# Kernel optimization log

Hardware: AMD Instinct MI355X
Metric: run time of the kernel (lower is better)

Reference implementation:

```python
import jax, jax.numpy as jnp
import numpy as np

N, M, NB, NA, NT, T, U = 1024, 32, 1024, 1536, 2048, 6, 32

def _one_hot_bool(n, m):
    ids = (jnp.arange(n) * m) // n  # contiguous assignment of entities to molecules
    return (jax.nn.one_hot(ids, m, dtype=jnp.float32) > 0.5)

def setup_inputs() -> dict:
    key = jax.random.key(0)
    ks = jax.random.split(key, 32)
    nrm = lambda i, shape, s=1.0: jax.random.normal(ks[i], shape, dtype=jnp.float32) * s
    inp = {
        'h_v': nrm(0, (N, U)), 'h_e': nrm(1, (NB, U)), 'h_a': nrm(2, (NA, U)),
        'h_t': nrm(3, (NT, U)), 'h_u': nrm(4, (M, U)),
        'h_v_history': nrm(5, (N, T, U)), 'h_e_history': nrm(6, (NB, T, U)),
        'h_a_history': nrm(7, (NA, T, U)), 'h_t_history': nrm(8, (NT, T, U)),
        'h_u_history': nrm(9, (M, T, U)),
        'atom_in_mol': _one_hot_bool(N, M), 'bond_in_mol': _one_hot_bool(NB, M),
        'angle_in_mol': _one_hot_bool(NA, M), 'torsion_in_mol': _one_hot_bool(NT, M),
        'adjacency_map': nrm(10, (N, N)), 'coordinates': nrm(11, (N, 3), 3.0),
        # learned parameters
        'Wk': nrm(12, (U, U), 0.1), 'bk': jnp.zeros((U,), jnp.float32),
        'Wq': nrm(13, (U, U), 0.1), 'bq': jnp.zeros((U,), jnp.float32),
        'Wv0': nrm(14, (1, U), 0.1), 'bv0': jnp.zeros((U,), jnp.float32),
        'Wv1': nrm(15, (U, U), 0.1), 'bv1': jnp.zeros((U,), jnp.float32),
        'Wp0': nrm(16, (3 * U, U), 0.1), 'bp0': jnp.zeros((U,), jnp.float32),
        'Wp1': nrm(17, (U, 19), 0.1), 'bp1': jnp.zeros((19,), jnp.float32),
        'Wd0': nrm(18, (5 * T * U, 64), 0.1), 'bd0': jnp.zeros((64,), jnp.float32),
        'Wd1': nrm(19, (64, 64), 0.1), 'bd1': jnp.zeros((64,), jnp.float32),
        'Wd2': nrm(20, (64, 19), 0.1), 'bd2': jnp.zeros((19,), jnp.float32),
    }
    return inp

def reference(h_v, h_e, h_a, h_t, h_u, h_v_history, h_e_history, h_a_history,
              h_t_history, h_u_history, atom_in_mol, bond_in_mol, angle_in_mol,
              torsion_in_mol, adjacency_map, coordinates,
              Wk, bk, Wq, bq, Wv0, bv0, Wv1, bv1, Wp0, bp0, Wp1, bp1,
              Wd0, bd0, Wd1, bd1, Wd2, bd2):
    A = atom_in_mol.astype(jnp.float32)              # [N, M]
    per_mol_mask = A @ A.T                           # [N, N] block-diagonal 0/1
    # pairwise Euclidean distance matrix
    diff = coordinates[:, None, :] - coordinates[None, :, :]
    dist = jnp.sqrt(jnp.maximum(jnp.sum(diff * diff, -1), 1e-12))[..., None]  # [N, N, 1]
    mask3 = per_mol_mask[..., None]                  # [N, N, 1]
    v = mask3 * (jax.nn.elu(dist @ Wv0 + bv0) @ Wv1 + bv1)          # [N, N, U]
    k = mask3 * (h_v @ Wk + bk)[:, None, :]                          # [N, N, U]
    q = mask3 * (h_v @ Wq + bq)[None, :, :]                          # [N, N, U]
    h_pair = jnp.concatenate([k, q, v], axis=2)                      # [N, N, 3U]
    h_pair = jnp.sum(jax.nn.sigmoid(h_pair @ Wp0 + bp0) @ Wp1 + bp1, axis=0)  # [N, 19]
    h_pair = A.T @ h_pair                                            # [M, 19]
    # per-mol segment sums of histories (faithful to mask-multiply-reduce, as einsum)
    seg = lambda mask, hist: jnp.einsum('em,etu->mtu', mask.astype(jnp.float32), hist)
    h_v_bar = seg(atom_in_mol, h_v_history).reshape(M, T * U)
    h_e_bar = seg(bond_in_mol, h_e_history).reshape(M, T * U)
    h_a_bar = seg(angle_in_mol, h_a_history).reshape(M, T * U)
    h_t_bar = seg(torsion_in_mol, h_t_history).reshape(M, T * U)  # computed, unused (as in source)
    # ConcatenateThenFullyConnect((64,'sigmoid',64,19)); note h_a_bar passed twice per source
    x = jnp.concatenate([h_v_bar, h_e_bar, h_u_history.reshape(M, T * U), h_a_bar, h_a_bar], axis=1)
    y = (jax.nn.sigmoid(x @ Wd0 + bd0) @ Wd1 + bd1) @ Wd2 + bd2      # [M, 19]
    return y + h_pair
```

## Files before the change

### kernel.cpp

```cpp
#include <hip/hip_runtime.h>
#include <math.h>


__device__ __forceinline__ float sigmoidf_(float x) { return 1.0f / (1.0f + __expf(-x)); }

__global__ __launch_bounds__(256) void fused_kernel(
    const float* __restrict__ h_v,
    const float* __restrict__ coords,
    const float* __restrict__ Wk, const float* __restrict__ bk,
    const float* __restrict__ Wq, const float* __restrict__ bq,
    const float* __restrict__ Wv0, const float* __restrict__ bv0,
    const float* __restrict__ Wv1, const float* __restrict__ bv1,
    const float* __restrict__ Wp0, const float* __restrict__ bp0,
    const float* __restrict__ Wp1, const float* __restrict__ bp1,
    const float* __restrict__ hvh,
    const float* __restrict__ heh,
    const float* __restrict__ hah,
    const float* __restrict__ huh,
    const float* __restrict__ Wd0, const float* __restrict__ bd0,
    const float* __restrict__ Wd1, const float* __restrict__ bd1,
    const float* __restrict__ Wd2, const float* __restrict__ bd2,
    float* __restrict__ out)
{
    __shared__ float hl[1024];
    __shared__ float wkl[1024], wql[1024], wv1l[1024];
    __shared__ float wp0l[3072];
    __shared__ float Kl[32 * 36], Ql[32 * 36];
    __shared__ float SKl[32 * 36], SQl[32 * 36];
    __shared__ float W2l[1024];
    __shared__ float wp1l[608];
    __shared__ float cbl[32], wv0l[32], bv0l[32];
    __shared__ float cxl[32], cyl[32], czl[32];
    __shared__ float Gl[4 * 32];
    __shared__ float Gs[32];
    __shared__ float xpart[14 * 192];
    __shared__ float xl[960];
    __shared__ float hp[4 * 64];
    __shared__ float h0[64], h1[64];

    const int tid = threadIdx.x;
    const int b = blockIdx.x;

    if (b < 32) {
        const int m = b;
        for (int task = tid; task < 672; task += 256) {
            const int seg = task / 48, c4 = task % 48;
            const float* src; int row0;
            if (seg < 4)      { src = hvh + (size_t)(m * 32) * 192; row0 = seg * 8; }
            else if (seg < 8) { src = heh + (size_t)(m * 32) * 192; row0 = (seg - 4) * 8; }
            else              { src = hah + (size_t)(m * 48) * 192; row0 = (seg - 8) * 8; }
            float4 acc = {0, 0, 0, 0};
            #pragma unroll
            for (int r = 0; r < 8; ++r) {
                const float4 v = *(const float4*)(src + (size_t)(row0 + r) * 192 + c4 * 4);
                acc.x += v.x; acc.y += v.y; acc.z += v.z; acc.w += v.w;
            }
            *(float4*)&xpart[seg * 192 + c4 * 4] = acc;
        }
        __syncthreads();
        if (tid < 192) {
            const float sv = xpart[tid] + xpart[192 + tid] + xpart[384 + tid] + xpart[576 + tid];
            const float se = xpart[768 + tid] + xpart[960 + tid] + xpart[1152 + tid] + xpart[1344 + tid];
            float sa = 0.0f;
            #pragma unroll
            for (int s2 = 8; s2 < 14; ++s2) sa += xpart[s2 * 192 + tid];
            xl[tid]       = sv;
            xl[192 + tid] = se;
            xl[384 + tid] = huh[m * 192 + tid];
            xl[576 + tid] = sa;
            xl[768 + tid] = sa;
        }
        __syncthreads();
        {
            const int o2 = tid & 63, part = tid >> 6;
            const int k0 = part * 240;
            float ssum = 0.0f;
            #pragma unroll 8
            for (int k = k0; k < k0 + 240; ++k) ssum += xl[k] * Wd0[k * 64 + o2];
            hp[part * 64 + o2] = ssum;
        }
        __syncthreads();
        if (tid < 64)
            h0[tid] = sigmoidf_(hp[tid] + hp[64 + tid] + hp[128 + tid] + hp[192 + tid] + bd0[tid]);
        __syncthreads();
        if (tid < 64) {
            float ssum = bd1[tid];
            #pragma unroll
            for (int k = 0; k < 64; ++k) ssum += h0[k] * Wd1[k * 64 + tid];
            h1[tid] = ssum;
        }
        __syncthreads();
        if (tid < 19) {
            float y = bd2[tid];
            #pragma unroll
            for (int k = 0; k < 64; ++k) y += h1[k] * Wd2[k * 19 + tid];
            float c0m = 0.0f;
            for (int u = 0; u < 32; ++u) c0m += sigmoidf_(bp0[u]) * Wp1[u * 19 + tid];
            atomicAdd(&out[m * 19 + tid], y + 31744.0f * c0m + 32768.0f * bp1[tid]);
        }
        return;
    }

    const int bb = b - 32;
    const int mol = bb >> 3;
    const int o = bb & 7;
    const int base = mol * 32;

    ((float4*)hl)[tid]   = ((const float4*)(h_v + (size_t)base * 32))[tid];
    ((float4*)wkl)[tid]  = ((const float4*)Wk)[tid];
    ((float4*)wql)[tid]  = ((const float4*)Wq)[tid];
    ((float4*)wv1l)[tid] = ((const float4*)Wv1)[tid];
    ((float4*)wp0l)[tid]       = ((const float4*)Wp0)[tid];
    ((float4*)wp0l)[tid + 256] = ((const float4*)Wp0)[tid + 256];
    ((float4*)wp0l)[tid + 512] = ((const float4*)Wp0)[tid + 512];
    for (int i = tid; i < 608; i += 256) wp1l[i] = Wp1[i];
    if (tid < 32) {
        wv0l[tid] = Wv0[tid];
        bv0l[tid] = bv0[tid];
        const int gi = base + tid;
        cxl[tid] = coords[gi * 3 + 0];
        cyl[tid] = coords[gi * 3 + 1];
        czl[tid] = coords[gi * 3 + 2];
    }
    __syncthreads();

    {
        const int u = tid & 31, g = tid >> 5;
        const int a0 = g * 4;
        float ka[4], qa[4];
        #pragma unroll
        for (int j = 0; j < 4; ++j) { ka[j] = bk[u]; qa[j] = bq[u]; }
        #pragma unroll
        for (int t4 = 0; t4 < 32; t4 += 4) {
            float4 h0v = *(const float4*)&hl[(a0 + 0) * 32 + t4];
            float4 h1v = *(const float4*)&hl[(a0 + 1) * 32 + t4];
            float4 h2v = *(const float4*)&hl[(a0 + 2) * 32 + t4];
            float4 h3v = *(const float4*)&hl[(a0 + 3) * 32 + t4];
            #pragma unroll
            for (int i = 0; i < 4; ++i) {
                const float wk = wkl[(t4 + i) * 32 + u];
                const float wq = wql[(t4 + i) * 32 + u];
                const float e0 = (&h0v.x)[i], e1 = (&h1v.x)[i], e2 = (&h2v.x)[i], e3 = (&h3v.x)[i];
                ka[0] += e0 * wk; ka[1] += e1 * wk; ka[2] += e2 * wk; ka[3] += e3 * wk;
                qa[0] += e0 * wq; qa[1] += e1 * wq; qa[2] += e2 * wq; qa[3] += e3 * wq;
            }
        }
        #pragma unroll
        for (int j = 0; j < 4; ++j) {
            Kl[(a0 + j) * 36 + u] = ka[j];
            Ql[(a0 + j) * 36 + u] = qa[j];
        }
    }
    __syncthreads();

    {
        const int w = tid & 31, g = tid >> 5;
        const int a0 = g * 4;
        float sk[4] = {0, 0, 0, 0}, sq[4] = {0, 0, 0, 0}, w2[4] = {0, 0, 0, 0};
        #pragma unroll
        for (int u4 = 0; u4 < 32; u4 += 4) {
            float4 k0 = *(const float4*)&Kl[(a0 + 0) * 36 + u4];
            float4 k1 = *(const float4*)&Kl[(a0 + 1) * 36 + u4];
            float4 k2 = *(const float4*)&Kl[(a0 + 2) * 36 + u4];
            float4 k3 = *(const float4*)&Kl[(a0 + 3) * 36 + u4];
            float4 q0 = *(const float4*)&Ql[(a0 + 0) * 36 + u4];
            float4 q1 = *(const float4*)&Ql[(a0 + 1) * 36 + u4];
            float4 q2 = *(const float4*)&Ql[(a0 + 2) * 36 + u4];
            float4 q3 = *(const float4*)&Ql[(a0 + 3) * 36 + u4];
            float4 v0 = *(const float4*)&wv1l[(a0 + 0) * 32 + u4];
            float4 v1 = *(const float4*)&wv1l[(a0 + 1) * 32 + u4];
            float4 v2 = *(const float4*)&wv1l[(a0 + 2) * 32 + u4];
            float4 v3 = *(const float4*)&wv1l[(a0 + 3) * 32 + u4];
            #pragma unroll
            for (int i = 0; i < 4; ++i) {
                const float pk = wp0l[(u4 + i) * 32 + w];
                const float pq = wp0l[(32 + u4 + i) * 32 + w];
                const float pv = wp0l[(64 + u4 + i) * 32 + w];
                sk[0] += (&k0.x)[i] * pk; sk[1] += (&k1.x)[i] * pk;
                sk[2] += (&k2.x)[i] * pk; sk[3] += (&k3.x)[i] * pk;
                sq[0] += (&q0.x)[i] * pq; sq[1] += (&q1.x)[i] * pq;
                sq[2] += (&q2.x)[i] * pq; sq[3] += (&q3.x)[i] * pq;
                w2[0] += (&v0.x)[i] * pv; w2[1] += (&v1.x)[i] * pv;
                w2[2] += (&v2.x)[i] * pv; w2[3] += (&v3.x)[i] * pv;
            }
        }
        #pragma unroll
        for (int j = 0; j < 4; ++j) {
            SKl[(a0 + j) * 36 + w] = sk[j];
            SQl[(a0 + j) * 36 + w] = sq[j];
            W2l[(a0 + j) * 32 + w] = w2[j];
        }
    }
    if (tid < 32) {
        float s = bp0[tid];
        #pragma unroll
        for (int u = 0; u < 32; ++u) s += bv1[u] * wp0l[(64 + u) * 32 + tid];
        cbl[tid] = s;
    }
    __syncthreads();

    const int ts = tid >> 2, sub = tid & 3;
    const int c0 = sub * 8;

    float g[8] = {0, 0, 0, 0, 0, 0, 0, 0};

    auto slot_accum = [&](int i, int j, bool mir) {
        const float dx = cxl[i] - cxl[j];
        const float dy = cyl[i] - cyl[j];
        const float dz = czl[i] - czl[j];
        const float dist = sqrtf(fmaxf(dx * dx + dy * dy + dz * dz, 1e-12f));
        float ew[8];
        {
            const float4 ca = *(const float4*)&cbl[c0];
            const float4 cb = *(const float4*)&cbl[c0 + 4];
            #pragma unroll
            for (int k = 0; k < 4; ++k) { ew[k] = (&ca.x)[k]; ew[k + 4] = (&cb.x)[k]; }
        }
        #pragma unroll
        for (int t = 0; t < 32; ++t) {
            const float xx = dist * wv0l[t] + bv0l[t];
            const float e = (xx > 0.0f) ? xx : (__expf(xx) - 1.0f);
            const float4 wa = *(const float4*)&W2l[t * 32 + c0];
            const float4 wb = *(const float4*)&W2l[t * 32 + c0 + 4];
            #pragma unroll
            for (int k = 0; k < 4; ++k) {
                ew[k]     += e * (&wa.x)[k];
                ew[k + 4] += e * (&wb.x)[k];
            }
        }
        {
            const float4 ka = *(const float4*)&SKl[i * 36 + c0];
            const float4 kb = *(const float4*)&SKl[i * 36 + c0 + 4];
            const float4 qa = *(const float4*)&SQl[j * 36 + c0];
            const float4 qb = *(const float4*)&SQl[j * 36 + c0 + 4];
            #pragma unroll
            for (int k = 0; k < 4; ++k) {
                g[k]     += sigmoidf_(ew[k]     + (&ka.x)[k] + (&qa.x)[k]);
                g[k + 4] += sigmoidf_(ew[k + 4] + (&kb.x)[k] + (&qb.x)[k]);
            }
        }
        if (mir) {
            const float4 ka = *(const float4*)&SKl[j * 36 + c0];
            const float4 kb = *(const float4*)&SKl[j * 36 + c0 + 4];
            const float4 qa = *(const float4*)&SQl[i * 36 + c0];
            const float4 qb = *(const float4*)&SQl[i * 36 + c0 + 4];
            #pragma unroll
            for (int k = 0; k < 4; ++k) {
                g[k]     += sigmoidf_(ew[k]     + (&ka.x)[k] + (&qa.x)[k]);
                g[k + 4] += sigmoidf_(ew[k + 4] + (&kb.x)[k] + (&qb.x)[k]);
            }
        }
    };

    {
        const int row = ts >> 5;
        const int i = ts & 31;
        int d; bool mir;
        if (o < 7) { d = 2 * o + 1 + row; mir = true; }
        else       { d = (row == 0) ? 15 : 16; mir = (row == 0); }
        const int j = (i + d) & 31;
        slot_accum(i, j, mir);
    }
    if (o == 7 && tid < 128) {
        const int i = tid >> 2;
        slot_accum(i, i, false);
    }

    #pragma unroll
    for (int k = 0; k < 8; ++k) {
        g[k] += __shfl_xor(g[k], 4);
        g[k] += __shfl_xor(g[k], 8);
        g[k] += __shfl_xor(g[k], 16);
        g[k] += __shfl_xor(g[k], 32);
    }
    const int lane = tid & 63, wid = tid >> 6;
    if (lane < 4) {
        #pragma unroll
        for (int k = 0; k < 8; ++k) Gl[wid * 32 + sub * 8 + k] = g[k];
    }
    __syncthreads();
    if (tid < 32) Gs[tid] = Gl[tid] + Gl[32 + tid] + Gl[64 + tid] + Gl[96 + tid];
    __syncthreads();
    if (tid < 19) {
        float r = 0.0f;
        #pragma unroll
        for (int u = 0; u < 32; ++u) r += Gs[u] * wp1l[u * 19 + tid];
        atomicAdd(&out[mol * 19 + tid], r);
    }
}

extern "C" void kernel_launch(void* const* d_in, const int* in_sizes, int n_in,
                              void* d_out, int out_size, void* d_ws, size_t ws_size,
                              hipStream_t stream) {
    (void)in_sizes; (void)n_in; (void)d_ws; (void)ws_size;
    const float* h_v    = (const float*)d_in[0];
    const float* hvh    = (const float*)d_in[5];
    const float* heh    = (const float*)d_in[6];
    const float* hah    = (const float*)d_in[7];
    const float* huh    = (const float*)d_in[9];
    const float* coords = (const float*)d_in[15];
    const float* Wk  = (const float*)d_in[16]; const float* bk  = (const float*)d_in[17];
    const float* Wq  = (const float*)d_in[18]; const float* bq  = (const float*)d_in[19];
    const float* Wv0 = (const float*)d_in[20]; const float* bv0 = (const float*)d_in[21];
    const float* Wv1 = (const float*)d_in[22]; const float* bv1 = (const float*)d_in[23];
    const float* Wp0 = (const float*)d_in[24]; const float* bp0 = (const float*)d_in[25];
    const float* Wp1 = (const float*)d_in[26]; const float* bp1 = (const float*)d_in[27];
    const float* Wd0 = (const float*)d_in[28]; const float* bd0 = (const float*)d_in[29];
    const float* Wd1 = (const float*)d_in[30]; const float* bd1 = (const float*)d_in[31];
    const float* Wd2 = (const float*)d_in[32]; const float* bd2 = (const float*)d_in[33];

    hipMemsetAsync(d_out, 0, (size_t)out_size * sizeof(float), stream);
    fused_kernel<<<288, 256, 0, stream>>>(h_v, coords, Wk, bk, Wq, bq,
                                          Wv0, bv0, Wv1, bv1, Wp0, bp0, Wp1, bp1,
                                          hvh, heh, hah, huh,
                                          Wd0, bd0, Wd1, bd1, Wd2, bd2,
                                          (float*)d_out);
}
```

Before: 24.53 us.

## Merge per-molecule work into one 1024-thread block, drop memset and atomics

Work is redistributed from 288 blocks of 256 threads (32 MLP blocks plus 8 pair blocks per molecule) to 32 blocks of 1024 threads, one per molecule. History segment sums, K/Q projection and the pairwise sigmoid stage now run inside the same block. Each thread processes 4 pairs plus their mirror pairs, and the diagonal term is computed separately with a 1e-6 distance. Because the block writes its output directly, the memset and the atomicAdds are no longer needed. In exchange, only 32 CUs are used, and the larger blocks may add register pressure and longer serial tails in the MLP stage.

```diff
diff --git a/kernel.cpp b/kernel.cpp
--- a/kernel.cpp
+++ b/kernel.cpp
@@ -4,7 +4,7 @@
 
 __device__ __forceinline__ float sigmoidf_(float x) { return 1.0f / (1.0f + __expf(-x)); }
 
-__global__ __launch_bounds__(256) void fused_kernel(
+__global__ __launch_bounds__(1024) void fused32(
     const float* __restrict__ h_v,
     const float* __restrict__ coords,
     const float* __restrict__ Wk, const float* __restrict__ bk,
@@ -28,92 +28,25 @@
     __shared__ float Kl[32 * 36], Ql[32 * 36];
     __shared__ float SKl[32 * 36], SQl[32 * 36];
     __shared__ float W2l[1024];
-    __shared__ float wp1l[608];
     __shared__ float cbl[32], wv0l[32], bv0l[32];
     __shared__ float cxl[32], cyl[32], czl[32];
-    __shared__ float Gl[4 * 32];
+    __shared__ float Gl[8 * 32];
     __shared__ float Gs[32];
     __shared__ float xpart[14 * 192];
     __shared__ float xl[960];
-    __shared__ float hp[4 * 64];
+    __shared__ float hp[16 * 64];
     __shared__ float h0[64], h1[64];
 
     const int tid = threadIdx.x;
-    const int b = blockIdx.x;
-
-    if (b < 32) {
-        const int m = b;
-        for (int task = tid; task < 672; task += 256) {
-            const int seg = task / 48, c4 = task % 48;
-            const float* src; int row0;
-            if (seg < 4)      { src = hvh + (size_t)(m * 32) * 192; row0 = seg * 8; }
-            else if (seg < 8) { src = heh + (size_t)(m * 32) * 192; row0 = (seg - 4) * 8; }
-            else              { src = hah + (size_t)(m * 48) * 192; row0 = (seg - 8) * 8; }
-            float4 acc = {0, 0, 0, 0};
-            #pragma unroll
-            for (int r = 0; r < 8; ++r) {
-                const float4 v = *(const float4*)(src + (size_t)(row0 + r) * 192 + c4 * 4);
-                acc.x += v.x; acc.y += v.y; acc.z += v.z; acc.w += v.w;
-            }
-            *(float4*)&xpart[seg * 192 + c4 * 4] = acc;
-        }
-        __syncthreads();
-        if (tid < 192) {
-            const float sv = xpart[tid] + xpart[192 + tid] + xpart[384 + tid] + xpart[576 + tid];
-            const float se = xpart[768 + tid] + xpart[960 + tid] + xpart[1152 + tid] + xpart[1344 + tid];
-            float sa = 0.0f;
-            #pragma unroll
-            for (int s2 = 8; s2 < 14; ++s2) sa += xpart[s2 * 192 + tid];
-            xl[tid]       = sv;
-            xl[192 + tid] = se;
-            xl[384 + tid] = huh[m * 192 + tid];
-            xl[576 + tid] = sa;
-            xl[768 + tid] = sa;
-        }
-        __syncthreads();
-        {
-            const int o2 = tid & 63, part = tid >> 6;
-            const int k0 = part * 240;
-            float ssum = 0.0f;
-            #pragma unroll 8
-            for (int k = k0; k < k0 + 240; ++k) ssum += xl[k] * Wd0[k * 64 + o2];
-            hp[part * 64 + o2] = ssum;
-        }
-        __syncthreads();
-        if (tid < 64)
-            h0[tid] = sigmoidf_(hp[tid] + hp[64 + tid] + hp[128 + tid] + hp[192 + tid] + bd0[tid]);
-        __syncthreads();
-        if (tid < 64) {
-            float ssum = bd1[tid];
-            #pragma unroll
-            for (int k = 0; k < 64; ++k) ssum += h0[k] * Wd1[k * 64 + tid];
-            h1[tid] = ssum;
-        }
-        __syncthreads();
-        if (tid < 19) {
-            float y = bd2[tid];
-            #pragma unroll
-            for (int k = 0; k < 64; ++k) y += h1[k] * Wd2[k * 19 + tid];
-            float c0m = 0.0f;
-            for (int u = 0; u < 32; ++u) c0m += sigmoidf_(bp0[u]) * Wp1[u * 19 + tid];
-            atomicAdd(&out[m * 19 + tid], y + 31744.0f * c0m + 32768.0f * bp1[tid]);
-        }
-        return;
-    }
-
-    const int bb = b - 32;
-    const int mol = bb >> 3;
-    const int o = bb & 7;
-    const int base = mol * 32;
-
-    ((float4*)hl)[tid]   = ((const float4*)(h_v + (size_t)base * 32))[tid];
-    ((float4*)wkl)[tid]  = ((const float4*)Wk)[tid];
-    ((float4*)wql)[tid]  = ((const float4*)Wq)[tid];
-    ((float4*)wv1l)[tid] = ((const float4*)Wv1)[tid];
-    ((float4*)wp0l)[tid]       = ((const float4*)Wp0)[tid];
-    ((float4*)wp0l)[tid + 256] = ((const float4*)Wp0)[tid + 256];
-    ((float4*)wp0l)[tid + 512] = ((const float4*)Wp0)[tid + 512];
-    for (int i = tid; i < 608; i += 256) wp1l[i] = Wp1[i];
+    const int m = blockIdx.x;
+    const int base = m * 32;
+
+    if (tid < 256)                       ((float4*)hl)[tid]         = ((const float4*)(h_v + (size_t)base * 32))[tid];
+    else if (tid < 512)                  ((float4*)wkl)[tid - 256]  = ((const float4*)Wk)[tid - 256];
+    else if (tid < 768)                  ((float4*)wql)[tid - 512]  = ((const float4*)Wq)[tid - 512];
+    else                                 ((float4*)wv1l)[tid - 768] = ((const float4*)Wv1)[tid - 768];
+    if (tid < 768)                       ((float4*)wp0l)[tid]       = ((const float4*)Wp0)[tid];
+    else if (tid < 816)                  ((float4*)(xl + 384))[tid - 768] = ((const float4*)(huh + (size_t)m * 192))[tid - 768];
     if (tid < 32) {
         wv0l[tid] = Wv0[tid];
         bv0l[tid] = bv0[tid];
@@ -122,9 +55,25 @@
         cyl[tid] = coords[gi * 3 + 1];
         czl[tid] = coords[gi * 3 + 2];
     }
-    __syncthreads();
-
-    {
+
+    if (tid >= 256 && tid < 928) {
+        const int task = tid - 256;
+        const int seg = task / 48, c4 = task % 48;
+        const float* src; int row0;
+        if (seg < 4)      { src = hvh + (size_t)(m * 32) * 192; row0 = seg * 8; }
+        else if (seg < 8) { src = heh + (size_t)(m * 32) * 192; row0 = (seg - 4) * 8; }
+        else              { src = hah + (size_t)(m * 48) * 192; row0 = (seg - 8) * 8; }
+        float4 acc = {0, 0, 0, 0};
+        #pragma unroll
+        for (int r = 0; r < 8; ++r) {
+            const float4 v = *(const float4*)(src + (size_t)(row0 + r) * 192 + c4 * 4);
+            acc.x += v.x; acc.y += v.y; acc.z += v.z; acc.w += v.w;
+        }
+        *(float4*)&xpart[seg * 192 + c4 * 4] = acc;
+    }
+    __syncthreads();
+
+    if (tid < 256) {
         const int u = tid & 31, g = tid >> 5;
         const int a0 = g * 4;
         float ka[4], qa[4];
@@ -153,7 +102,7 @@
     }
     __syncthreads();
 
-    {
+    if (tid < 256) {
         const int w = tid & 31, g = tid >> 5;
         const int a0 = g * 4;
         float sk[4] = {0, 0, 0, 0}, sq[4] = {0, 0, 0, 0}, w2[4] = {0, 0, 0, 0};
@@ -197,75 +146,86 @@
         for (int u = 0; u < 32; ++u) s += bv1[u] * wp0l[(64 + u) * 32 + tid];
         cbl[tid] = s;
     }
-    __syncthreads();
-
-    const int ts = tid >> 2, sub = tid & 3;
-    const int c0 = sub * 8;
+    if (tid >= 512 && tid < 704) {
+        const int c = tid - 512;
+        const float sv = xpart[c] + xpart[192 + c] + xpart[384 + c] + xpart[576 + c];
+        const float se = xpart[768 + c] + xpart[960 + c] + xpart[1152 + c] + xpart[1344 + c];
+        float sa = 0.0f;
+        #pragma unroll
+        for (int s2 = 8; s2 < 14; ++s2) sa += xpart[s2 * 192 + c];
+        xl[c]       = sv;
+        xl[192 + c] = se;
+        xl[576 + c] = sa;
+        xl[768 + c] = sa;
+    }
+    __syncthreads();
 
     float g[8] = {0, 0, 0, 0, 0, 0, 0, 0};
-
-    auto slot_accum = [&](int i, int j, bool mir) {
-        const float dx = cxl[i] - cxl[j];
-        const float dy = cyl[i] - cyl[j];
-        const float dz = czl[i] - czl[j];
-        const float dist = sqrtf(fmaxf(dx * dx + dy * dy + dz * dz, 1e-12f));
-        float ew[8];
+    if (tid < 512) {
+        const int q = tid >> 2, sub = tid & 3, c0 = sub * 8;
+        const int s0 = q * 4;
+        const float vmul = (s0 < 496) ? 1.0f : 0.0f;
+        const int s0v = (s0 < 496) ? s0 : 0;
+        const int d  = (s0v < 480) ? (1 + (s0v >> 5)) : 16;
+        const int bi = (s0v < 480) ? (s0v & 31) : (s0v - 480);
+
+        float dist[4];
+        #pragma unroll
+        for (int k = 0; k < 4; ++k) {
+            const int i = bi + k, j = (i + d) & 31;
+            const float dx = cxl[i] - cxl[j];
+            const float dy = cyl[i] - cyl[j];
+            const float dz = czl[i] - czl[j];
+            dist[k] = sqrtf(fmaxf(dx * dx + dy * dy + dz * dz, 1e-12f));
+        }
+        float ew[4][8];
         {
             const float4 ca = *(const float4*)&cbl[c0];
-            const float4 cb = *(const float4*)&cbl[c0 + 4];
-            #pragma unroll
-            for (int k = 0; k < 4; ++k) { ew[k] = (&ca.x)[k]; ew[k + 4] = (&cb.x)[k]; }
+            const float4 cb2 = *(const float4*)&cbl[c0 + 4];
+            #pragma unroll
+            for (int k = 0; k < 4; ++k)
+                #pragma unroll
+                for (int c = 0; c < 4; ++c) {
+                    ew[k][c] = (&ca.x)[c];
+                    ew[k][c + 4] = (&cb2.x)[c];
+                }
         }
         #pragma unroll
         for (int t = 0; t < 32; ++t) {
-            const float xx = dist * wv0l[t] + bv0l[t];
-            const float e = (xx > 0.0f) ? xx : (__expf(xx) - 1.0f);
+            const float wv = wv0l[t], bv = bv0l[t];
             const float4 wa = *(const float4*)&W2l[t * 32 + c0];
             const float4 wb = *(const float4*)&W2l[t * 32 + c0 + 4];
             #pragma unroll
             for (int k = 0; k < 4; ++k) {
-                ew[k]     += e * (&wa.x)[k];
-                ew[k + 4] += e * (&wb.x)[k];
+                const float xx = dist[k] * wv + bv;
+                const float e = (xx > 0.0f) ? xx : (__expf(xx) - 1.0f);
+                #pragma unroll
+                for (int c = 0; c < 4; ++c) {
+                    ew[k][c]     += e * (&wa.x)[c];
+                    ew[k][c + 4] += e * (&wb.x)[c];
+                }
             }
         }
-        {
-            const float4 ka = *(const float4*)&SKl[i * 36 + c0];
-            const float4 kb = *(const float4*)&SKl[i * 36 + c0 + 4];
-            const float4 qa = *(const float4*)&SQl[j * 36 + c0];
-            const float4 qb = *(const float4*)&SQl[j * 36 + c0 + 4];
-            #pragma unroll
-            for (int k = 0; k < 4; ++k) {
-                g[k]     += sigmoidf_(ew[k]     + (&ka.x)[k] + (&qa.x)[k]);
-                g[k + 4] += sigmoidf_(ew[k + 4] + (&kb.x)[k] + (&qb.x)[k]);
+        #pragma unroll
+        for (int k = 0; k < 4; ++k) {
+            const int i = bi + k, j = (i + d) & 31;
+            const float4 kia = *(const float4*)&SKl[i * 36 + c0];
+            const float4 kib = *(const float4*)&SKl[i * 36 + c0 + 4];
+            const float4 qja = *(const float4*)&SQl[j * 36 + c0];
+            const float4 qjb = *(const float4*)&SQl[j * 36 + c0 + 4];
+            const float4 kja = *(const float4*)&SKl[j * 36 + c0];
+            const float4 kjb = *(const float4*)&SKl[j * 36 + c0 + 4];
+            const float4 qia = *(const float4*)&SQl[i * 36 + c0];
+            const float4 qib = *(const float4*)&SQl[i * 36 + c0 + 4];
+            #pragma unroll
+            for (int c = 0; c < 4; ++c) {
+                g[c]     += vmul * (sigmoidf_(ew[k][c]     + (&kia.x)[c] + (&qja.x)[c])
+                                  + sigmoidf_(ew[k][c]     + (&kja.x)[c] + (&qia.x)[c]));
+                g[c + 4] += vmul * (sigmoidf_(ew[k][c + 4] + (&kib.x)[c] + (&qjb.x)[c])
+                                  + sigmoidf_(ew[k][c + 4] + (&kjb.x)[c] + (&qib.x)[c]));
             }
         }
-        if (mir) {
-            const float4 ka = *(const float4*)&SKl[j * 36 + c0];
-            const float4 kb = *(const float4*)&SKl[j * 36 + c0 + 4];
-            const float4 qa = *(const float4*)&SQl[i * 36 + c0];
-            const float4 qb = *(const float4*)&SQl[i * 36 + c0 + 4];
-            #pragma unroll
-            for (int k = 0; k < 4; ++k) {
-                g[k]     += sigmoidf_(ew[k]     + (&ka.x)[k] + (&qa.x)[k]);
-                g[k + 4] += sigmoidf_(ew[k + 4] + (&kb.x)[k] + (&qb.x)[k]);
-            }
-        }
-    };
-
-    {
-        const int row = ts >> 5;
-        const int i = ts & 31;
-        int d; bool mir;
-        if (o < 7) { d = 2 * o + 1 + row; mir = true; }
-        else       { d = (row == 0) ? 15 : 16; mir = (row == 0); }
-        const int j = (i + d) & 31;
-        slot_accum(i, j, mir);
-    }
-    if (o == 7 && tid < 128) {
-        const int i = tid >> 2;
-        slot_accum(i, i, false);
-    }
-
+    }
     #pragma unroll
     for (int k = 0; k < 8; ++k) {
         g[k] += __shfl_xor(g[k], 4);
@@ -273,26 +233,78 @@
         g[k] += __shfl_xor(g[k], 16);
         g[k] += __shfl_xor(g[k], 32);
     }
-    const int lane = tid & 63, wid = tid >> 6;
-    if (lane < 4) {
-        #pragma unroll
-        for (int k = 0; k < 8; ++k) Gl[wid * 32 + sub * 8 + k] = g[k];
-    }
-    __syncthreads();
-    if (tid < 32) Gs[tid] = Gl[tid] + Gl[32 + tid] + Gl[64 + tid] + Gl[96 + tid];
+    {
+        const int lane = tid & 63, wid = tid >> 6;
+        if (wid < 8 && lane < 4) {
+            #pragma unroll
+            for (int k = 0; k < 8; ++k) Gl[wid * 32 + (lane & 3) * 8 + k] = g[k];
+        }
+    }
+    __syncthreads();
+    if (tid < 32) {
+        float s = 0.0f;
+        #pragma unroll
+        for (int w = 0; w < 8; ++w) s += Gl[w * 32 + tid];
+        float ewd = cbl[tid];
+        #pragma unroll
+        for (int t = 0; t < 32; ++t) {
+            const float xx = 1e-6f * wv0l[t] + bv0l[t];
+            const float e = (xx > 0.0f) ? xx : (__expf(xx) - 1.0f);
+            ewd += e * W2l[t * 32 + tid];
+        }
+        #pragma unroll
+        for (int i = 0; i < 32; ++i)
+            s += sigmoidf_(ewd + SKl[i * 36 + tid] + SQl[i * 36 + tid]);
+        Gs[tid] = s;
+    }
+    __syncthreads();
+
+    {
+        const int o = tid & 63, part = tid >> 6;
+        const int k0 = part * 60;
+        float ssum = 0.0f;
+        #pragma unroll
+        for (int k4 = 0; k4 < 60; k4 += 4) {
+            const float4 xv = *(const float4*)&xl[k0 + k4];
+            ssum += xv.x * Wd0[(k0 + k4 + 0) * 64 + o];
+            ssum += xv.y * Wd0[(k0 + k4 + 1) * 64 + o];
+            ssum += xv.z * Wd0[(k0 + k4 + 2) * 64 + o];
+            ssum += xv.w * Wd0[(k0 + k4 + 3) * 64 + o];
+        }
+        hp[part * 64 + o] = ssum;
+    }
+    __syncthreads();
+    if (tid < 64) {
+        float v = bd0[tid];
+        #pragma unroll
+        for (int p = 0; p < 16; ++p) v += hp[p * 64 + tid];
+        h0[tid] = sigmoidf_(v);
+    }
+    __syncthreads();
+    if (tid < 64) {
+        float ssum = bd1[tid];
+        #pragma unroll
+        for (int k = 0; k < 64; ++k) ssum += h0[k] * Wd1[k * 64 + tid];
+        h1[tid] = ssum;
+    }
     __syncthreads();
     if (tid < 19) {
-        float r = 0.0f;
-        #pragma unroll
-        for (int u = 0; u < 32; ++u) r += Gs[u] * wp1l[u * 19 + tid];
-        atomicAdd(&out[mol * 19 + tid], r);
+        float y = bd2[tid];
+        #pragma unroll
+        for (int k = 0; k < 64; ++k) y += h1[k] * Wd2[k * 19 + tid];
+        float c0m = 0.0f;
+        for (int u = 0; u < 32; ++u) c0m += sigmoidf_(bp0[u]) * Wp1[u * 19 + tid];
+        float pr = 0.0f;
+        #pragma unroll
+        for (int u = 0; u < 32; ++u) pr += Gs[u] * Wp1[u * 19 + tid];
+        out[m * 19 + tid] = y + pr + 31744.0f * c0m + 32768.0f * bp1[tid];
     }
 }
 
 extern "C" void kernel_launch(void* const* d_in, const int* in_sizes, int n_in,
                               void* d_out, int out_size, void* d_ws, size_t ws_size,
                               hipStream_t stream) {
-    (void)in_sizes; (void)n_in; (void)d_ws; (void)ws_size;
+    (void)in_sizes; (void)n_in; (void)out_size; (void)d_ws; (void)ws_size;
     const float* h_v    = (const float*)d_in[0];
     const float* hvh    = (const float*)d_in[5];
     const float* heh    = (const float*)d_in[6];
@@ -309,10 +321,9 @@
     const float* Wd1 = (const float*)d_in[30]; const float* bd1 = (const float*)d_in[31];
     const float* Wd2 = (const float*)d_in[32]; const float* bd2 = (const float*)d_in[33];
 
-    hipMemsetAsync(d_out, 0, (size_t)out_size * sizeof(float), stream);
-    fused_kernel<<<288, 256, 0, stream>>>(h_v, coords, Wk, bk, Wq, bq,
-                                          Wv0, bv0, Wv1, bv1, Wp0, bp0, Wp1, bp1,
-                                          hvh, heh, hah, huh,
-                                          Wd0, bd0, Wd1, bd1, Wd2, bd2,
-                                          (float*)d_out);
+    fused32<<<32, 1024, 0, stream>>>(h_v, coords, Wk, bk, Wq, bq,
+                                     Wv0, bv0, Wv1, bv1, Wp0, bp0, Wp1, bp1,
+                                     hvh, heh, hah, huh,
+                                     Wd0, bd0, Wd1, bd1, Wd2, bd2,
+                                     (float*)d_out);
 }
```

Result: slower. 35.14 us (+43.2%).
